# Performance work log

Measured on AMD Instinct MI355X. Metric: run time of the kernel, lower is better.

The kernel has to match this reference:

```python
import jax, jax.numpy as jnp
import numpy as np

B, C, W, H, HEADS = 4, 512, 32, 32, 8
D = C // HEADS          # head dim = 64
N = W * H               # tokens = 1024


def setup_inputs() -> dict:
    key = jax.random.key(0)
    ks = jax.random.split(key, 11)
    s = 0.02
    return {
        "q1": jax.random.normal(ks[0], (B, C, W, H), jnp.float32),
        "q2": jax.random.normal(ks[1], (B, C, W, H), jnp.float32),
        "q3": jax.random.normal(ks[2], (B, C, W, H), jnp.float32),
        "Wq": jax.random.normal(ks[3], (C, C), jnp.float32) * s,
        "bq": jnp.zeros((C,), jnp.float32),
        "Wk": jax.random.normal(ks[4], (C, C), jnp.float32) * s,
        "bk": jnp.zeros((C,), jnp.float32),
        "Wv": jax.random.normal(ks[5], (C, C), jnp.float32) * s,
        "bv": jnp.zeros((C,), jnp.float32),
        # BoT-style relative position embeddings (broadcast over the grid)
        "rel_h": jax.random.normal(ks[6], (HEADS, D, 1, H), jnp.float32) * s,
        "rel_w": jax.random.normal(ks[7], (HEADS, D, W, 1), jnp.float32) * s,
    }


def reference(q1, q2, q3, Wq, bq, Wk, bk, Wv, bv, rel_h, rel_w):
    b, c, w, h = q1.shape
    heads = rel_h.shape[0]
    d = c // heads
    n = w * h

    def proj(x, Wm, bm):
        # 1x1 conv == channel matmul; then view (b, heads, d, n)
        y = jnp.einsum('oc,bchw->bohw', Wm, x) + bm[None, :, None, None]
        return y.reshape(b, heads, d, n)

    q = proj(q1, Wq, bq)
    k = proj(q2, Wk, bk)
    v = proj(q3, Wv, bv)

    # (heads, d, w, h) -> (heads, d, n); used transposed as (heads, n, d)
    pos = (rel_h + rel_w).reshape(heads, d, n)

    def branch(a, bmat, outv):
        # energy = a^T bmat + pos^T a ; softmax over last dim; out = outv @ attn^T
        energy = (jnp.einsum('bhdn,bhdm->bhnm', a, bmat)
                  + jnp.einsum('hdn,bhdm->bhnm', pos, a))
        attn = jax.nn.softmax(energy, axis=-1)  # (b, heads, n, n)
        out = jnp.einsum('bhdm,bhnm->bhdn', outv, attn)
        return out.reshape(b, c, w, h)

    out_q = branch(q, k, v)   # energy_q = q^T k + pos^T q ; out = v @ attn_q^T
    out_k = branch(k, v, q)   # energy_k = k^T v + pos^T k ; out = q @ attn_k^T
    out_v = branch(v, q, k)   # energy_v = v^T q + pos^T v ; out = k @ attn_v^T

    return jnp.concatenate((out_q, out_k, out_v), axis=0)
```

## Files before the change

### kernel.cpp

```cpp
#include <hip/hip_runtime.h>

typedef __attribute__((ext_vector_type(8))) __bf16 bf16x8;
typedef __attribute__((ext_vector_type(4))) float f32x4;
typedef __attribute__((ext_vector_type(4))) int i32x4;
typedef __attribute__((ext_vector_type(2))) int i32x2;
typedef __attribute__((ext_vector_type(4))) unsigned short u16x4;
typedef __attribute__((ext_vector_type(8))) unsigned short u16x8;
typedef unsigned short u16;
typedef unsigned int u32;

#define DEVI __device__ __forceinline__

constexpr int CB = 4;
constexpr int CC = 512;
constexpr int CH = 8;
constexpr int CD = 64;
constexpr int CN = 1024;
constexpr float L2E = 1.44269504088896f;

DEVI u16 f2bf(float f) {
    u32 u = __builtin_bit_cast(u32, f);
    u = (u + 0x7FFFu + ((u >> 16) & 1u)) >> 16;
    return (u16)u;
}
DEVI float bf2f(u16 u) {
    return __builtin_bit_cast(float, (u32)u << 16);
}
DEVI u16 f2bf_c(float f) {
    return __builtin_bit_cast(u16, (__bf16)f);
}
DEVI float exp2_fast(float x) {
    float r;
    asm("v_exp_f32 %0, %1" : "=v"(r) : "v"(x));
    return r;
}

DEVI int swzA(int row, int col16) {
    return (row * 256 + col16 * 16) ^ ((row & 7) << 4);
}
DEVI int swzB(int row, int col16) {
    return (row * 128 + col16 * 16) ^ ((row & 7) << 4);
}

DEVI bf16x8 ldfrag(const u16* base, int byteoff) {
    const i32x4* p = reinterpret_cast<const i32x4*>(reinterpret_cast<const char*>(base) + byteoff);
    return __builtin_bit_cast(bf16x8, *p);
}
DEVI void st8(u16* base, int byteoff, i32x2 v) {
    *reinterpret_cast<i32x2*>(reinterpret_cast<char*>(base) + byteoff) = v;
}
DEVI void async16(u16* lds, const u16* g) {
    __builtin_amdgcn_global_load_lds(
        (const __attribute__((address_space(1))) unsigned int*)g,
        (__attribute__((address_space(3))) unsigned int*)lds,
        16, 0, 0);
}

__global__ __launch_bounds__(256) void mqf_convx_kernel(
    const float* __restrict__ q1, const float* __restrict__ q2, const float* __restrict__ q3,
    const float* __restrict__ Wq, const float* __restrict__ Wk, const float* __restrict__ Wv,
    u16* __restrict__ XT, u16* __restrict__ Wbf)
{
    __shared__ u16 T[64 * 66];
    const int t = threadIdx.x;
    const int n0 = blockIdx.x * 64, c0 = blockIdx.y * 64;
    const int p = blockIdx.z >> 2, b = blockIdx.z & 3;
    const float* X = (p == 0 ? q1 : p == 1 ? q2 : q3) + (size_t)b * CC * CN;
    u16* dst = XT + (size_t)(p * CB + b) * CN * CC;

    if (t < 128) {
        int bid = blockIdx.x + (blockIdx.y << 4) + (blockIdx.z << 7);
        int idx = (bid * 128 + t) * 4;
        int pw = idx >> 18;
        int off = idx & 0x3FFFF;
        const float* W = (pw == 0 ? Wq : pw == 1 ? Wk : Wv);
        f32x4 v = *reinterpret_cast<const f32x4*>(W + off);
        u16x4 pk;
        #pragma unroll
        for (int j = 0; j < 4; ++j) pk[j] = f2bf(v[j]);
        *reinterpret_cast<u16x4*>(Wbf + idx) = pk;
    }

    #pragma unroll
    for (int pass = 0; pass < 4; ++pass) {
        int idx = pass * 256 + t;
        int cl = idx >> 4, nl = (idx & 15) * 4;
        f32x4 v = *reinterpret_cast<const f32x4*>(X + (size_t)(c0 + cl) * CN + n0 + nl);
        u32 lo = (u32)f2bf(v[0]) | ((u32)f2bf(v[1]) << 16);
        u32 hi = (u32)f2bf(v[2]) | ((u32)f2bf(v[3]) << 16);
        *reinterpret_cast<u32*>(&T[cl * 66 + nl]) = lo;
        *reinterpret_cast<u32*>(&T[cl * 66 + nl + 2]) = hi;
    }
    __syncthreads();
    #pragma unroll
    for (int pass = 0; pass < 2; ++pass) {
        int idx = pass * 256 + t;
        int nl = idx >> 3, g = idx & 7;
        u16x8 pk;
        #pragma unroll
        for (int j = 0; j < 8; ++j) pk[j] = T[(g * 8 + j) * 66 + nl];
        *reinterpret_cast<u16x8*>(dst + (size_t)(n0 + nl) * CC + c0 + g * 8) = pk;
    }
}

__global__ __launch_bounds__(256) void mqf_gemm_kernel(
    const u16* __restrict__ Wbf, const u16* __restrict__ XT,
    const float* __restrict__ bq, const float* __restrict__ bk, const float* __restrict__ bv,
    u16* __restrict__ projN, u16* __restrict__ projT)
{
    __shared__ __align__(16) char lds_raw[49152];
    u16* At0 = (u16*)lds_raw;
    u16* At1 = At0 + 4096;
    u16* Bt0 = At0 + 8192;
    u16* Bt1 = Bt0 + 8192;
    float* Tb = (float*)lds_raw;

    const int t = threadIdx.x;
    const int w = t >> 6, l = t & 63;
    const int li = l & 15, hi = l >> 4;

    int id = blockIdx.x + (blockIdx.y << 3) + (blockIdx.z << 6);
    int nid = (id & 7) * 96 + (id >> 3);
    const int n0 = (nid & 7) * 128;
    const int o0 = ((nid >> 3) & 7) * 64;
    const int pb = nid >> 6;
    const int p = pb >> 2, b = pb & 3;

    const u16* A = Wbf + (size_t)p * CC * CC;
    const u16* B = XT + (size_t)(p * CB + b) * CN * CC;
    const float* bm = (p == 0 ? bq : p == 1 ? bk : bv);
    u16* oN = projN + (size_t)(p * CB + b) * CC * CN;
    u16* oT = projT + (size_t)(p * CB + b) * CN * CC;

    const int sj = t & 7;

    auto issueDMA = [&](int step, u16* AtW, u16* BtW) {
        int c0 = step * 64;
        #pragma unroll
        for (int q = 0; q < 2; ++q) {
            int idx = q * 256 + t;
            int row = idx >> 3;
            int col = (sj ^ (row & 7)) * 8;
            async16(AtW + idx * 8, A + (size_t)(o0 + row) * CC + c0 + col);
        }
        #pragma unroll
        for (int q = 0; q < 4; ++q) {
            int idx = q * 256 + t;
            int row = idx >> 3;
            int col = (sj ^ (row & 7)) * 8;
            async16(BtW + idx * 8, B + (size_t)(n0 + row) * CC + c0 + col);
        }
    };

    const f32x4 fz = {0.f, 0.f, 0.f, 0.f};
    f32x4 acc[4][2];
    #pragma unroll
    for (int m = 0; m < 4; ++m)
        #pragma unroll
        for (int s = 0; s < 2; ++s) acc[m][s] = fz;

    issueDMA(0, At0, Bt0);
    __syncthreads();

    for (int step = 0; step < 8; ++step) {
        u16* AtC = (step & 1) ? At1 : At0;
        u16* BtC = (step & 1) ? Bt1 : Bt0;
        if (step < 7) issueDMA(step + 1, (step & 1) ? At0 : At1, (step & 1) ? Bt0 : Bt1);

        __builtin_amdgcn_s_setprio(1);
        #pragma unroll
        for (int kk = 0; kk < 2; ++kk) {
            bf16x8 af[4], bfr[2];
            #pragma unroll
            for (int m = 0; m < 4; ++m)
                af[m] = ldfrag(AtC, swzB(m * 16 + li, kk * 4 + hi));
            #pragma unroll
            for (int s = 0; s < 2; ++s)
                bfr[s] = ldfrag(BtC, swzB(w * 32 + s * 16 + li, kk * 4 + hi));
            #pragma unroll
            for (int m = 0; m < 4; ++m)
                #pragma unroll
                for (int s = 0; s < 2; ++s)
                    acc[m][s] = __builtin_amdgcn_mfma_f32_16x16x32_bf16(af[m], bfr[s], acc[m][s], 0, 0, 0);
        }
        __builtin_amdgcn_s_setprio(0);
        __syncthreads();
    }

    #pragma unroll
    for (int m = 0; m < 4; ++m) {
        #pragma unroll
        for (int r = 0; r < 4; ++r) {
            int orow = m * 16 + hi * 4 + r;
            float bias = bm[o0 + orow];
            #pragma unroll
            for (int s = 0; s < 2; ++s)
                Tb[orow * 129 + w * 32 + s * 16 + li] = acc[m][s][r] + bias;
        }
    }
    __syncthreads();
    {
        int row = t >> 2, nbase = (t & 3) * 32;
        #pragma unroll
        for (int j = 0; j < 4; ++j) {
            u16x8 pk;
            #pragma unroll
            for (int i = 0; i < 8; ++i) pk[i] = f2bf_c(Tb[row * 129 + nbase + j * 8 + i]);
            *reinterpret_cast<u16x8*>(oN + (size_t)(o0 + row) * CN + n0 + nbase + j * 8) = pk;
        }
        int nrow = t >> 1, obase = (t & 1) * 32;
        #pragma unroll
        for (int j = 0; j < 4; ++j) {
            u16x8 pk;
            #pragma unroll
            for (int i = 0; i < 8; ++i) pk[i] = f2bf_c(Tb[(obase + j * 8 + i) * 129 + nrow]);
            *reinterpret_cast<u16x8*>(oT + (size_t)(n0 + nrow) * CC + o0 + obase + j * 8) = pk;
        }
    }
}

__global__ __launch_bounds__(256, 3) void mqf_attn_kernel(
    const u16* __restrict__ projN, const u16* __restrict__ projT,
    const float* __restrict__ rel_h, const float* __restrict__ rel_w,
    float* __restrict__ out)
{
    __shared__ __align__(16) u16 Kt[2][64 * 128];
    __shared__ __align__(16) u16 Vt[2][64 * 64];

    const int t = threadIdx.x;
    const int w = t >> 6, l = t & 63;
    const int li = l & 15, hi = l >> 4;

    int id = blockIdx.x + (blockIdx.y << 3) + (blockIdx.z << 8);
    int nid = (id & 7) * 96 + (id >> 3);
    const int n0 = (nid & 7) * 128;
    const int by = (nid >> 3) & 31;
    const int br = nid >> 8;
    const int b = by >> 3, h = by & 7;

    const int ai = br, bi = (br + 1) % 3, vi = (br + 2) % 3;
    const size_t tsz = (size_t)CB * CC * CN;
    const u16* aT = projT + ai * tsz + (size_t)b * CN * CC;
    const u16* bT = projT + bi * tsz + (size_t)b * CN * CC;
    const u16* vN = projN + vi * tsz + (size_t)b * CC * CN;

    bf16x8 qf[2][4];
    #pragma unroll
    for (int g = 0; g < 2; ++g) {
        const int nq = n0 + (w * 2 + g) * 16 + li;
        #pragma unroll
        for (int kk = 0; kk < 2; ++kk) {
            u16x8 raw = *reinterpret_cast<const u16x8*>(
                aT + (size_t)nq * CC + h * CD + kk * 32 + hi * 8);
            u16x8 pk;
            #pragma unroll
            for (int j = 0; j < 8; ++j) pk[j] = f2bf_c(bf2f(raw[j]) * L2E);
            qf[g][kk] = __builtin_bit_cast(bf16x8, pk);
        }
        #pragma unroll
        for (int kk = 2; kk < 4; ++kk) {
            u16x8 pk;
            #pragma unroll
            for (int j = 0; j < 8; ++j) {
                int d = (kk - 2) * 32 + hi * 8 + j;
                float f = rel_h[(h * CD + d) * 32 + (nq & 31)]
                        + rel_w[(h * CD + d) * 32 + (nq >> 5)];
                pk[j] = f2bf_c(f * L2E);
            }
            qf[g][kk] = __builtin_bit_cast(bf16x8, pk);
        }
    }

    const f32x4 fz = {0.f, 0.f, 0.f, 0.f};
    f32x4 oacc[2][4];
    #pragma unroll
    for (int g = 0; g < 2; ++g)
        #pragma unroll
        for (int dg = 0; dg < 4; ++dg) oacc[g][dg] = fz;
    float lsum[2] = {0.f, 0.f};

    i32x4 vreg[2];
    const int vrow = t >> 3, vc = (t & 7) * 8;
    const int vb0 = ((vc >> 5) << 6) + (((vc >> 2) & 3) << 4) + (((vc >> 4) & 1) << 3);

    auto loadV = [&](int m1) {
        const u16* rv = vN + (size_t)(h * CD + vrow) * CN + m1;
        vreg[0] = *reinterpret_cast<const i32x4*>(rv + vc);
        vreg[1] = *reinterpret_cast<const i32x4*>(rv + (size_t)32 * CN + vc);
    };
    auto writeV = [&](u16* VtW) {
        i32x2 lo0 = {vreg[0][0], vreg[0][1]}, hi0 = {vreg[0][2], vreg[0][3]};
        int r0 = vrow, r1 = vrow + 32;
        st8(VtW, (r0 * 128 + vb0) ^ ((r0 & 7) << 4), lo0);
        st8(VtW, (r0 * 128 + vb0 + 16) ^ ((r0 & 7) << 4), hi0);
        i32x2 lo1 = {vreg[1][0], vreg[1][1]}, hi1 = {vreg[1][2], vreg[1][3]};
        st8(VtW, (r1 * 128 + vb0) ^ ((r1 & 7) << 4), lo1);
        st8(VtW, (r1 * 128 + vb0 + 16) ^ ((r1 & 7) << 4), hi1);
    };
    auto issueKdma = [&](int m1, u16* KtW) {
        #pragma unroll
        for (int i = 0; i < 4; ++i) {
            int row = w * 16 + i * 4 + hi;
            int col16 = li ^ (row & 7);
            const u16* src = ((li & 8) ? aT : bT)
                + (size_t)(m1 + row) * CC + h * CD + (col16 & 7) * 8;
            async16(KtW + w * 2048 + i * 512 + l * 8, src);
        }
    };

    loadV(0);
    writeV(Vt[0]);
    issueKdma(0, Kt[0]);
    loadV(64);
    __syncthreads();

    for (int tt = 0; tt < 16; ++tt) {
        if (tt < 15) {
            writeV(Vt[(tt + 1) & 1]);
            issueKdma((tt + 1) * 64, Kt[(tt + 1) & 1]);
        }
        if (tt < 14) loadV((tt + 2) * 64);

        const u16* KtC = Kt[tt & 1];
        const u16* VtC = Vt[tt & 1];

        f32x4 e[2][4];
        #pragma unroll
        for (int s = 0; s < 4; ++s) { e[0][s] = fz; e[1][s] = fz; }
        __builtin_amdgcn_s_setprio(1);
        #pragma unroll
        for (int kk = 0; kk < 4; ++kk) {
            #pragma unroll
            for (int s = 0; s < 2; ++s) {
                bf16x8 af = ldfrag(KtC, swzA(s * 16 + li, kk * 4 + hi));
                e[0][s] = __builtin_amdgcn_mfma_f32_16x16x32_bf16(af, qf[0][kk], e[0][s], 0, 0, 0);
                e[1][s] = __builtin_amdgcn_mfma_f32_16x16x32_bf16(af, qf[1][kk], e[1][s], 0, 0, 0);
            }
        }
        #pragma unroll
        for (int kk = 0; kk < 4; ++kk) {
            #pragma unroll
            for (int s = 2; s < 4; ++s) {
                bf16x8 af = ldfrag(KtC, swzA(s * 16 + li, kk * 4 + hi));
                e[0][s] = __builtin_amdgcn_mfma_f32_16x16x32_bf16(af, qf[0][kk], e[0][s], 0, 0, 0);
                e[1][s] = __builtin_amdgcn_mfma_f32_16x16x32_bf16(af, qf[1][kk], e[1][s], 0, 0, 0);
            }
        }
        __builtin_amdgcn_s_setprio(0);

        bf16x8 pa0[2], pa1[2];
        #pragma unroll
        for (int g = 0; g < 2; ++g) {
            float ts = 0.f;
            u16x8 pk;
            #pragma unroll
            for (int r = 0; r < 4; ++r) {
                float p0 = exp2_fast(e[g][0][r]);
                float p1 = exp2_fast(e[g][1][r]);
                ts += p0 + p1;
                pk[r] = f2bf_c(p0);
                pk[4 + r] = f2bf_c(p1);
            }
            lsum[g] += ts;
            pa0[g] = __builtin_bit_cast(bf16x8, pk);
        }
        __builtin_amdgcn_s_setprio(1);
        #pragma unroll
        for (int dg = 0; dg < 4; ++dg) {
            bf16x8 vf = ldfrag(VtC, swzB(dg * 16 + li, hi));
            oacc[0][dg] = __builtin_amdgcn_mfma_f32_16x16x32_bf16(vf, pa0[0], oacc[0][dg], 0, 0, 0);
            oacc[1][dg] = __builtin_amdgcn_mfma_f32_16x16x32_bf16(vf, pa0[1], oacc[1][dg], 0, 0, 0);
        }
        __builtin_amdgcn_s_setprio(0);
        #pragma unroll
        for (int g = 0; g < 2; ++g) {
            float ts = 0.f;
            u16x8 pk;
            #pragma unroll
            for (int r = 0; r < 4; ++r) {
                float p0 = exp2_fast(e[g][2][r]);
                float p1 = exp2_fast(e[g][3][r]);
                ts += p0 + p1;
                pk[r] = f2bf_c(p0);
                pk[4 + r] = f2bf_c(p1);
            }
            lsum[g] += ts;
            pa1[g] = __builtin_bit_cast(bf16x8, pk);
        }
        __builtin_amdgcn_s_setprio(1);
        #pragma unroll
        for (int dg = 0; dg < 4; ++dg) {
            bf16x8 vf = ldfrag(VtC, swzB(dg * 16 + li, 4 + hi));
            oacc[0][dg] = __builtin_amdgcn_mfma_f32_16x16x32_bf16(vf, pa1[0], oacc[0][dg], 0, 0, 0);
            oacc[1][dg] = __builtin_amdgcn_mfma_f32_16x16x32_bf16(vf, pa1[1], oacc[1][dg], 0, 0, 0);
        }
        __builtin_amdgcn_s_setprio(0);
        __syncthreads();
    }

    #pragma unroll
    for (int g = 0; g < 2; ++g) {
        float lt = lsum[g];
        lt += __shfl_xor(lt, 16, 64);
        lt += __shfl_xor(lt, 32, 64);
        float inv = 1.f / lt;
        float* outp = out + ((size_t)(br * CB + b) * CC + h * CD) * CN
                    + n0 + (w * 2 + g) * 16 + li;
        #pragma unroll
        for (int dg = 0; dg < 4; ++dg) {
            #pragma unroll
            for (int r = 0; r < 4; ++r) {
                int drow = dg * 16 + hi * 4 + r;
                outp[(size_t)drow * CN] = oacc[g][dg][r] * inv;
            }
        }
    }
}

extern "C" void kernel_launch(void* const* d_in, const int* in_sizes, int n_in,
                              void* d_out, int out_size, void* d_ws, size_t ws_size,
                              hipStream_t stream) {
    const float* q1 = (const float*)d_in[0];
    const float* q2 = (const float*)d_in[1];
    const float* q3 = (const float*)d_in[2];
    const float* Wq = (const float*)d_in[3];
    const float* bq = (const float*)d_in[4];
    const float* Wk = (const float*)d_in[5];
    const float* bk = (const float*)d_in[6];
    const float* Wv = (const float*)d_in[7];
    const float* bv = (const float*)d_in[8];
    const float* rh = (const float*)d_in[9];
    const float* rw = (const float*)d_in[10];

    u16* XT    = (u16*)d_ws;
    u16* Wbf   = XT + (size_t)3 * CB * CN * CC;
    u16* projN = Wbf + (size_t)3 * CC * CC;
    u16* projT = projN + (size_t)3 * CB * CC * CN;
    float* outp = (float*)d_out;

    dim3 gc(CN / 64, CC / 64, 12);
    mqf_convx_kernel<<<gc, 256, 0, stream>>>(q1, q2, q3, Wq, Wk, Wv, XT, Wbf);
    dim3 gg(CN / 128, CC / 64, 12);
    mqf_gemm_kernel<<<gg, 256, 0, stream>>>(Wbf, XT, bq, bk, bv, projN, projT);
    dim3 ga(CN / 128, CB * CH, 3);
    mqf_attn_kernel<<<ga, 256, 0, stream>>>(projN, projT, rh, rw, outp);
}
```

Before: 72.58 us.

## Shrink attention blocks to 128 threads and 32-key tiles for more blocks

The attention kernel now uses 2-wave blocks covering 64 queries instead of 4-wave blocks covering 128, doubling the grid. Each K/V tile shrinks from 64 to 32 keys, so the loop runs 32 iterations, and a new V LDS swizzle and a K DMA mapping fit the smaller tiles. The aim is better CU occupancy and load balance on a grid that was small for the hardware, with half the LDS per block. The cost is more barriers and loop iterations per block, plus less reuse of each loaded K/V tile.

```diff
diff --git a/kernel.cpp b/kernel.cpp
--- a/kernel.cpp
+++ b/kernel.cpp
@@ -40,6 +40,9 @@
 }
 DEVI int swzB(int row, int col16) {
     return (row * 128 + col16 * 16) ^ ((row & 7) << 4);
+}
+DEVI int swzV(int row, int u) {
+    return row * 64 + ((u ^ (row & 3)) << 4);
 }
 
 DEVI bf16x8 ldfrag(const u16* base, int byteoff) {
@@ -219,23 +222,23 @@
     }
 }
 
-__global__ __launch_bounds__(256, 3) void mqf_attn_kernel(
+__global__ __launch_bounds__(128, 3) void mqf_attn_kernel(
     const u16* __restrict__ projN, const u16* __restrict__ projT,
     const float* __restrict__ rel_h, const float* __restrict__ rel_w,
     float* __restrict__ out)
 {
-    __shared__ __align__(16) u16 Kt[2][64 * 128];
-    __shared__ __align__(16) u16 Vt[2][64 * 64];
+    __shared__ __align__(16) u16 Kt[2][32 * 128];
+    __shared__ __align__(16) u16 Vt[2][64 * 32];
 
     const int t = threadIdx.x;
     const int w = t >> 6, l = t & 63;
     const int li = l & 15, hi = l >> 4;
 
-    int id = blockIdx.x + (blockIdx.y << 3) + (blockIdx.z << 8);
-    int nid = (id & 7) * 96 + (id >> 3);
-    const int n0 = (nid & 7) * 128;
-    const int by = (nid >> 3) & 31;
-    const int br = nid >> 8;
+    int id = blockIdx.x + (blockIdx.y << 4) + (blockIdx.z << 9);
+    int nid = (id & 7) * 192 + (id >> 3);
+    const int n0 = (nid & 15) * 64;
+    const int by = (nid >> 4) & 31;
+    const int br = nid >> 9;
     const int b = by >> 3, h = by & 7;
 
     const int ai = br, bi = (br + 1) % 3, vi = (br + 2) % 3;
@@ -280,53 +283,52 @@
     float lsum[2] = {0.f, 0.f};
 
     i32x4 vreg[2];
-    const int vrow = t >> 3, vc = (t & 7) * 8;
-    const int vb0 = ((vc >> 5) << 6) + (((vc >> 2) & 3) << 4) + (((vc >> 4) & 1) << 3);
+    const int vd = t >> 1, seg = t & 1, vc = seg * 16;
+    const int uA = (vc >> 2) & 3;
+    const int boff = (vc >> 4) * 8;
 
     auto loadV = [&](int m1) {
-        const u16* rv = vN + (size_t)(h * CD + vrow) * CN + m1;
-        vreg[0] = *reinterpret_cast<const i32x4*>(rv + vc);
-        vreg[1] = *reinterpret_cast<const i32x4*>(rv + (size_t)32 * CN + vc);
+        const u16* rv = vN + (size_t)(h * CD + vd) * CN + m1 + vc;
+        vreg[0] = *reinterpret_cast<const i32x4*>(rv);
+        vreg[1] = *reinterpret_cast<const i32x4*>(rv + 8);
     };
     auto writeV = [&](u16* VtW) {
-        i32x2 lo0 = {vreg[0][0], vreg[0][1]}, hi0 = {vreg[0][2], vreg[0][3]};
-        int r0 = vrow, r1 = vrow + 32;
-        st8(VtW, (r0 * 128 + vb0) ^ ((r0 & 7) << 4), lo0);
-        st8(VtW, (r0 * 128 + vb0 + 16) ^ ((r0 & 7) << 4), hi0);
-        i32x2 lo1 = {vreg[1][0], vreg[1][1]}, hi1 = {vreg[1][2], vreg[1][3]};
-        st8(VtW, (r1 * 128 + vb0) ^ ((r1 & 7) << 4), lo1);
-        st8(VtW, (r1 * 128 + vb0 + 16) ^ ((r1 & 7) << 4), hi1);
+        i32x2 a0 = {vreg[0][0], vreg[0][1]}, a1 = {vreg[0][2], vreg[0][3]};
+        i32x2 b0 = {vreg[1][0], vreg[1][1]}, b1 = {vreg[1][2], vreg[1][3]};
+        st8(VtW, swzV(vd, uA + 0) + boff, a0);
+        st8(VtW, swzV(vd, uA + 1) + boff, a1);
+        st8(VtW, swzV(vd, uA + 2) + boff, b0);
+        st8(VtW, swzV(vd, uA + 3) + boff, b1);
     };
     auto issueKdma = [&](int m1, u16* KtW) {
         #pragma unroll
         for (int i = 0; i < 4; ++i) {
-            int row = w * 16 + i * 4 + hi;
+            int row = i * 8 + w * 4 + hi;
             int col16 = li ^ (row & 7);
-            const u16* src = ((li & 8) ? aT : bT)
+            const u16* src = ((col16 & 8) ? aT : bT)
                 + (size_t)(m1 + row) * CC + h * CD + (col16 & 7) * 8;
-            async16(KtW + w * 2048 + i * 512 + l * 8, src);
+            async16(KtW + (i * 128 + t) * 8, src);
         }
     };
 
     loadV(0);
     writeV(Vt[0]);
     issueKdma(0, Kt[0]);
-    loadV(64);
+    loadV(32);
     __syncthreads();
 
-    for (int tt = 0; tt < 16; ++tt) {
-        if (tt < 15) {
+    for (int tt = 0; tt < 32; ++tt) {
+        if (tt < 31) {
             writeV(Vt[(tt + 1) & 1]);
-            issueKdma((tt + 1) * 64, Kt[(tt + 1) & 1]);
-        }
-        if (tt < 14) loadV((tt + 2) * 64);
+            issueKdma((tt + 1) * 32, Kt[(tt + 1) & 1]);
+        }
+        if (tt < 30) loadV((tt + 2) * 32);
 
         const u16* KtC = Kt[tt & 1];
         const u16* VtC = Vt[tt & 1];
 
-        f32x4 e[2][4];
-        #pragma unroll
-        for (int s = 0; s < 4; ++s) { e[0][s] = fz; e[1][s] = fz; }
+        f32x4 e[2][2];
+        e[0][0] = fz; e[0][1] = fz; e[1][0] = fz; e[1][1] = fz;
         __builtin_amdgcn_s_setprio(1);
         #pragma unroll
         for (int kk = 0; kk < 4; ++kk) {
@@ -337,18 +339,9 @@
                 e[1][s] = __builtin_amdgcn_mfma_f32_16x16x32_bf16(af, qf[1][kk], e[1][s], 0, 0, 0);
             }
         }
-        #pragma unroll
-        for (int kk = 0; kk < 4; ++kk) {
-            #pragma unroll
-            for (int s = 2; s < 4; ++s) {
-                bf16x8 af = ldfrag(KtC, swzA(s * 16 + li, kk * 4 + hi));
-                e[0][s] = __builtin_amdgcn_mfma_f32_16x16x32_bf16(af, qf[0][kk], e[0][s], 0, 0, 0);
-                e[1][s] = __builtin_amdgcn_mfma_f32_16x16x32_bf16(af, qf[1][kk], e[1][s], 0, 0, 0);
-            }
-        }
         __builtin_amdgcn_s_setprio(0);
 
-        bf16x8 pa0[2], pa1[2];
+        bf16x8 pa[2];
         #pragma unroll
         for (int g = 0; g < 2; ++g) {
             float ts = 0.f;
@@ -362,37 +355,15 @@
                 pk[4 + r] = f2bf_c(p1);
             }
             lsum[g] += ts;
-            pa0[g] = __builtin_bit_cast(bf16x8, pk);
-        }
+            pa[g] = __builtin_bit_cast(bf16x8, pk);
+        }
+
         __builtin_amdgcn_s_setprio(1);
         #pragma unroll
         for (int dg = 0; dg < 4; ++dg) {
-            bf16x8 vf = ldfrag(VtC, swzB(dg * 16 + li, hi));
-            oacc[0][dg] = __builtin_amdgcn_mfma_f32_16x16x32_bf16(vf, pa0[0], oacc[0][dg], 0, 0, 0);
-            oacc[1][dg] = __builtin_amdgcn_mfma_f32_16x16x32_bf16(vf, pa0[1], oacc[1][dg], 0, 0, 0);
-        }
-        __builtin_amdgcn_s_setprio(0);
-        #pragma unroll
-        for (int g = 0; g < 2; ++g) {
-            float ts = 0.f;
-            u16x8 pk;
-            #pragma unroll
-            for (int r = 0; r < 4; ++r) {
-                float p0 = exp2_fast(e[g][2][r]);
-                float p1 = exp2_fast(e[g][3][r]);
-                ts += p0 + p1;
-                pk[r] = f2bf_c(p0);
-                pk[4 + r] = f2bf_c(p1);
-            }
-            lsum[g] += ts;
-            pa1[g] = __builtin_bit_cast(bf16x8, pk);
-        }
-        __builtin_amdgcn_s_setprio(1);
-        #pragma unroll
-        for (int dg = 0; dg < 4; ++dg) {
-            bf16x8 vf = ldfrag(VtC, swzB(dg * 16 + li, 4 + hi));
-            oacc[0][dg] = __builtin_amdgcn_mfma_f32_16x16x32_bf16(vf, pa1[0], oacc[0][dg], 0, 0, 0);
-            oacc[1][dg] = __builtin_amdgcn_mfma_f32_16x16x32_bf16(vf, pa1[1], oacc[1][dg], 0, 0, 0);
+            bf16x8 vf = ldfrag(VtC, swzV(dg * 16 + li, hi));
+            oacc[0][dg] = __builtin_amdgcn_mfma_f32_16x16x32_bf16(vf, pa[0], oacc[0][dg], 0, 0, 0);
+            oacc[1][dg] = __builtin_amdgcn_mfma_f32_16x16x32_bf16(vf, pa[1], oacc[1][dg], 0, 0, 0);
         }
         __builtin_amdgcn_s_setprio(0);
         __syncthreads();
@@ -442,6 +413,6 @@
     mqf_convx_kernel<<<gc, 256, 0, stream>>>(q1, q2, q3, Wq, Wk, Wv, XT, Wbf);
     dim3 gg(CN / 128, CC / 64, 12);
     mqf_gemm_kernel<<<gg, 256, 0, stream>>>(Wbf, XT, bq, bk, bv, projN, projT);
-    dim3 ga(CN / 128, CB * CH, 3);
-    mqf_attn_kernel<<<ga, 256, 0, stream>>>(projN, projT, rh, rw, outp);
-}
+    dim3 ga(CN / 64, CB * CH, 3);
+    mqf_attn_kernel<<<ga, 128, 0, stream>>>(projN, projT, rh, rw, outp);
+}
```

Result: slower. 79.78 us (+9.9%).

## Use two waves per attention block with 64 query rows per wave

Applied to the files above, without the earlier changes.

The attention kernel drops from 256 to 128 threads per block, and each wave now handles four 16-row query groups instead of two. Each K and V fragment read from LDS is reused across twice as many MFMAs, and the loads that stage K and V in LDS are spread over fewer threads. The cost is roughly double the accumulator and score registers per thread, with a lower launch-bounds occupancy target and fewer waves per block to hide latency.

```diff
diff --git a/kernel.cpp b/kernel.cpp
--- a/kernel.cpp
+++ b/kernel.cpp
@@ -219,7 +219,7 @@
     }
 }
 
-__global__ __launch_bounds__(256, 3) void mqf_attn_kernel(
+__global__ __launch_bounds__(128, 2) void mqf_attn_kernel(
     const u16* __restrict__ projN, const u16* __restrict__ projT,
     const float* __restrict__ rel_h, const float* __restrict__ rel_w,
     float* __restrict__ out)
@@ -244,10 +244,10 @@
     const u16* bT = projT + bi * tsz + (size_t)b * CN * CC;
     const u16* vN = projN + vi * tsz + (size_t)b * CC * CN;
 
-    bf16x8 qf[2][4];
-    #pragma unroll
-    for (int g = 0; g < 2; ++g) {
-        const int nq = n0 + (w * 2 + g) * 16 + li;
+    bf16x8 qf[4][4];
+    #pragma unroll
+    for (int g = 0; g < 4; ++g) {
+        const int nq = n0 + w * 64 + g * 16 + li;
         #pragma unroll
         for (int kk = 0; kk < 2; ++kk) {
             u16x8 raw = *reinterpret_cast<const u16x8*>(
@@ -272,39 +272,48 @@
     }
 
     const f32x4 fz = {0.f, 0.f, 0.f, 0.f};
-    f32x4 oacc[2][4];
-    #pragma unroll
-    for (int g = 0; g < 2; ++g)
+    f32x4 oacc[4][4];
+    #pragma unroll
+    for (int g = 0; g < 4; ++g)
         #pragma unroll
         for (int dg = 0; dg < 4; ++dg) oacc[g][dg] = fz;
-    float lsum[2] = {0.f, 0.f};
-
-    i32x4 vreg[2];
-    const int vrow = t >> 3, vc = (t & 7) * 8;
-    const int vb0 = ((vc >> 5) << 6) + (((vc >> 2) & 3) << 4) + (((vc >> 4) & 1) << 3);
+    float lsum[4] = {0.f, 0.f, 0.f, 0.f};
+
+    i32x4 vreg[4];
+    const int vrow = t >> 2, vc = (t & 3) * 16;
+    const int vb0 = ((vc >> 5) << 6) + (((vc >> 4) & 1) << 3);
 
     auto loadV = [&](int m1) {
-        const u16* rv = vN + (size_t)(h * CD + vrow) * CN + m1;
-        vreg[0] = *reinterpret_cast<const i32x4*>(rv + vc);
-        vreg[1] = *reinterpret_cast<const i32x4*>(rv + (size_t)32 * CN + vc);
+        const u16* rv = vN + (size_t)(h * CD + vrow) * CN + m1 + vc;
+        vreg[0] = *reinterpret_cast<const i32x4*>(rv);
+        vreg[1] = *reinterpret_cast<const i32x4*>(rv + 8);
+        vreg[2] = *reinterpret_cast<const i32x4*>(rv + (size_t)32 * CN);
+        vreg[3] = *reinterpret_cast<const i32x4*>(rv + (size_t)32 * CN + 8);
     };
     auto writeV = [&](u16* VtW) {
-        i32x2 lo0 = {vreg[0][0], vreg[0][1]}, hi0 = {vreg[0][2], vreg[0][3]};
-        int r0 = vrow, r1 = vrow + 32;
-        st8(VtW, (r0 * 128 + vb0) ^ ((r0 & 7) << 4), lo0);
-        st8(VtW, (r0 * 128 + vb0 + 16) ^ ((r0 & 7) << 4), hi0);
-        i32x2 lo1 = {vreg[1][0], vreg[1][1]}, hi1 = {vreg[1][2], vreg[1][3]};
-        st8(VtW, (r1 * 128 + vb0) ^ ((r1 & 7) << 4), lo1);
-        st8(VtW, (r1 * 128 + vb0 + 16) ^ ((r1 & 7) << 4), hi1);
+        #pragma unroll
+        for (int half = 0; half < 2; ++half) {
+            int r = vrow + half * 32;
+            int sw = (r & 7) << 4;
+            i32x2 a0 = {vreg[half * 2][0], vreg[half * 2][1]};
+            i32x2 a1 = {vreg[half * 2][2], vreg[half * 2][3]};
+            i32x2 b0 = {vreg[half * 2 + 1][0], vreg[half * 2 + 1][1]};
+            i32x2 b1 = {vreg[half * 2 + 1][2], vreg[half * 2 + 1][3]};
+            st8(VtW, (r * 128 + vb0) ^ sw, a0);
+            st8(VtW, (r * 128 + vb0 + 16) ^ sw, a1);
+            st8(VtW, (r * 128 + vb0 + 32) ^ sw, b0);
+            st8(VtW, (r * 128 + vb0 + 48) ^ sw, b1);
+        }
     };
     auto issueKdma = [&](int m1, u16* KtW) {
         #pragma unroll
-        for (int i = 0; i < 4; ++i) {
-            int row = w * 16 + i * 4 + hi;
-            int col16 = li ^ (row & 7);
-            const u16* src = ((li & 8) ? aT : bT)
+        for (int i = 0; i < 8; ++i) {
+            int u = i * 128 + t;
+            int row = u >> 4, cu = u & 15;
+            int col16 = cu ^ (row & 7);
+            const u16* src = ((col16 & 8) ? aT : bT)
                 + (size_t)(m1 + row) * CC + h * CD + (col16 & 7) * 8;
-            async16(KtW + w * 2048 + i * 512 + l * 8, src);
+            async16(KtW + u * 8, src);
         }
     };
 
@@ -324,17 +333,20 @@
         const u16* KtC = Kt[tt & 1];
         const u16* VtC = Vt[tt & 1];
 
-        f32x4 e[2][4];
-        #pragma unroll
-        for (int s = 0; s < 4; ++s) { e[0][s] = fz; e[1][s] = fz; }
+        f32x4 e[4][4];
+        #pragma unroll
+        for (int g = 0; g < 4; ++g)
+            #pragma unroll
+            for (int s = 0; s < 4; ++s) e[g][s] = fz;
         __builtin_amdgcn_s_setprio(1);
         #pragma unroll
         for (int kk = 0; kk < 4; ++kk) {
             #pragma unroll
             for (int s = 0; s < 2; ++s) {
                 bf16x8 af = ldfrag(KtC, swzA(s * 16 + li, kk * 4 + hi));
-                e[0][s] = __builtin_amdgcn_mfma_f32_16x16x32_bf16(af, qf[0][kk], e[0][s], 0, 0, 0);
-                e[1][s] = __builtin_amdgcn_mfma_f32_16x16x32_bf16(af, qf[1][kk], e[1][s], 0, 0, 0);
+                #pragma unroll
+                for (int g = 0; g < 4; ++g)
+                    e[g][s] = __builtin_amdgcn_mfma_f32_16x16x32_bf16(af, qf[g][kk], e[g][s], 0, 0, 0);
             }
         }
         #pragma unroll
@@ -342,15 +354,16 @@
             #pragma unroll
             for (int s = 2; s < 4; ++s) {
                 bf16x8 af = ldfrag(KtC, swzA(s * 16 + li, kk * 4 + hi));
-                e[0][s] = __builtin_amdgcn_mfma_f32_16x16x32_bf16(af, qf[0][kk], e[0][s], 0, 0, 0);
-                e[1][s] = __builtin_amdgcn_mfma_f32_16x16x32_bf16(af, qf[1][kk], e[1][s], 0, 0, 0);
+                #pragma unroll
+                for (int g = 0; g < 4; ++g)
+                    e[g][s] = __builtin_amdgcn_mfma_f32_16x16x32_bf16(af, qf[g][kk], e[g][s], 0, 0, 0);
             }
         }
         __builtin_amdgcn_s_setprio(0);
 
-        bf16x8 pa0[2], pa1[2];
-        #pragma unroll
-        for (int g = 0; g < 2; ++g) {
+        bf16x8 pa0[4], pa1[4];
+        #pragma unroll
+        for (int g = 0; g < 4; ++g) {
             float ts = 0.f;
             u16x8 pk;
             #pragma unroll
@@ -368,12 +381,13 @@
         #pragma unroll
         for (int dg = 0; dg < 4; ++dg) {
             bf16x8 vf = ldfrag(VtC, swzB(dg * 16 + li, hi));
-            oacc[0][dg] = __builtin_amdgcn_mfma_f32_16x16x32_bf16(vf, pa0[0], oacc[0][dg], 0, 0, 0);
-            oacc[1][dg] = __builtin_amdgcn_mfma_f32_16x16x32_bf16(vf, pa0[1], oacc[1][dg], 0, 0, 0);
+            #pragma unroll
+            for (int g = 0; g < 4; ++g)
+                oacc[g][dg] = __builtin_amdgcn_mfma_f32_16x16x32_bf16(vf, pa0[g], oacc[g][dg], 0, 0, 0);
         }
         __builtin_amdgcn_s_setprio(0);
         #pragma unroll
-        for (int g = 0; g < 2; ++g) {
+        for (int g = 0; g < 4; ++g) {
             float ts = 0.f;
             u16x8 pk;
             #pragma unroll
@@ -391,21 +405,22 @@
         #pragma unroll
         for (int dg = 0; dg < 4; ++dg) {
             bf16x8 vf = ldfrag(VtC, swzB(dg * 16 + li, 4 + hi));
-            oacc[0][dg] = __builtin_amdgcn_mfma_f32_16x16x32_bf16(vf, pa1[0], oacc[0][dg], 0, 0, 0);
-            oacc[1][dg] = __builtin_amdgcn_mfma_f32_16x16x32_bf16(vf, pa1[1], oacc[1][dg], 0, 0, 0);
+            #pragma unroll
+            for (int g = 0; g < 4; ++g)
+                oacc[g][dg] = __builtin_amdgcn_mfma_f32_16x16x32_bf16(vf, pa1[g], oacc[g][dg], 0, 0, 0);
         }
         __builtin_amdgcn_s_setprio(0);
         __syncthreads();
     }
 
     #pragma unroll
-    for (int g = 0; g < 2; ++g) {
+    for (int g = 0; g < 4; ++g) {
         float lt = lsum[g];
         lt += __shfl_xor(lt, 16, 64);
         lt += __shfl_xor(lt, 32, 64);
         float inv = 1.f / lt;
         float* outp = out + ((size_t)(br * CB + b) * CC + h * CD) * CN
-                    + n0 + (w * 2 + g) * 16 + li;
+                    + n0 + w * 64 + g * 16 + li;
         #pragma unroll
         for (int dg = 0; dg < 4; ++dg) {
             #pragma unroll
@@ -443,5 +458,5 @@
     dim3 gg(CN / 128, CC / 64, 12);
     mqf_gemm_kernel<<<gg, 256, 0, stream>>>(Wbf, XT, bq, bk, bv, projN, projT);
     dim3 ga(CN / 128, CB * CH, 3);
-    mqf_attn_kernel<<<ga, 256, 0, stream>>>(projN, projT, rh, rw, outp);
-}
+    mqf_attn_kernel<<<ga, 128, 0, stream>>>(projN, projT, rh, rw, outp);
+}
```

Result: slower. 138.5 us (+90.8%).
